# Kernel tuning notes

Hardware: AMD Instinct MI355X
Metric: run time of the kernel (lower is better)

## Reference

```python
import jax, jax.numpy as jnp
import numpy as np

K = 16          # neighbors used for attention (knn uses K+1 incl. self)
LRELU = 0.01    # torch LeakyReLU default negative_slope


def setup_inputs() -> dict:
    key = jax.random.key(0)
    ks = jax.random.split(key, 12)
    B, N = 4, 8192
    w = lambda k, shape: (jax.random.normal(k, shape, jnp.float32) * 0.05)
    inp = {
        "x": jax.random.normal(ks[0], (B, N, 3), jnp.float32),
        "global_feat": jax.random.normal(ks[1], (B, 1024), jnp.float32),  # unused by forward (matches source)
        # convs1 = MLP_CONV(3, [64,128]): Conv1d(3,64)+ReLU, Conv1d(64,128)
        "W1": w(ks[2], (64, 3)),    "b1": jnp.zeros((64,), jnp.float32),
        "W2": w(ks[3], (128, 64)),  "b2": jnp.zeros((128,), jnp.float32),
        # convs2: Conv2d(9,64,1x1)+LReLU, Conv2d(64,64,1x1)+LReLU, Conv2d(64,128,1x1)
        "Wc1": w(ks[4], (64, 9)),   "bc1": jnp.zeros((64,), jnp.float32),
        "Wc2": w(ks[5], (64, 64)),  "bc2": jnp.zeros((64,), jnp.float32),
        "Wc3": w(ks[6], (128, 64)), "bc3": jnp.zeros((128,), jnp.float32),
        # conv_query / conv_key: Conv2d(256,256,1x1)
        "Wq": w(ks[7], (256, 256)), "bq": jnp.zeros((256,), jnp.float32),
        "Wk": w(ks[8], (256, 256)), "bk": jnp.zeros((256,), jnp.float32),
    }
    return inp


def _lrelu(t):
    return jnp.where(t >= 0, t, LRELU * t)


def _forward(x, W1, b1, W2, b2, Wc1, bc1, Wc2, bc2, Wc3, bc3, Wq, bq, Wk, bk):
    # convs1: pointwise MLP on coords -> per-point features f [B,N,128]
    f = jax.nn.relu(jnp.einsum('bnc,oc->bno', x, W1) + b1)
    f = jnp.einsum('bnc,oc->bno', f, W2) + b2

    # knn_points(x, x, K=17): squared-distance matrix, nearest-first (self at slot 0)
    sq = jnp.sum(x * x, axis=-1)                              # [B,N]
    d2 = sq[:, :, None] + sq[:, None, :] - 2.0 * jnp.einsum('bnc,bmc->bnm', x, x)
    _, idx = jax.lax.top_k(-d2, K + 1)                        # [B,N,K+1]

    gather = jax.vmap(lambda a, i: a[i])                      # per-batch fancy gather
    knn_x = gather(x, idx)                                    # [B,N,K+1,3]
    knn_f = gather(f, idx)                                    # [B,N,K+1,128]

    rep = jnp.broadcast_to(x[:, :, None, :], knn_x.shape)     # repeat_x
    r = jnp.concatenate([rep, knn_x, rep - knn_x], axis=-1)   # [B,N,K+1,9]
    r = _lrelu(jnp.einsum('bnkc,oc->bnko', r, Wc1) + bc1)
    r = _lrelu(jnp.einsum('bnkc,oc->bnko', r, Wc2) + bc2)
    r = jnp.einsum('bnkc,oc->bnko', r, Wc3) + bc3             # [B,N,K+1,128]

    feat = jnp.concatenate([knn_f, r], axis=-1)               # [B,N,K+1,256]
    q = jnp.einsum('bnkc,oc->bnko', feat[:, :, :1, :], Wq) + bq   # [B,N,1,256]
    k = jnp.einsum('bnkc,oc->bnko', feat[:, :, 1:, :], Wk) + bk   # [B,N,K,256]
    w = jax.nn.softmax(jnp.sum(q * k, axis=-1), axis=-1)      # [B,N,K]
    new_x = jnp.sum(w[..., None] * knn_x[:, :, 1:, :], axis=2)    # [B,N,3]
    return new_x


def reference(x, global_feat, W1, b1, W2, b2, Wc1, bc1, Wc2, bc2, Wc3, bc3, Wq, bq, Wk, bk):
    del global_feat  # present in the torch signature but unused in forward
    return _forward(x, W1, b1, W2, b2, Wc1, bc1, Wc2, bc2, Wc3, bc3, Wq, bq, Wk, bk)
```

## Files before the change

kernel.cpp:

```cpp
#include <hip/hip_runtime.h>
#include <hip/hip_bf16.h>

#define NPTS 8192
#define NB   4

typedef unsigned short u16;
typedef unsigned int   u32;
typedef short bf16x8 __attribute__((ext_vector_type(8)));
typedef float f32x4  __attribute__((ext_vector_type(4)));

static __device__ __forceinline__ float bflo(u32 u){ return __uint_as_float(u << 16); }
static __device__ __forceinline__ float bfhi(u32 u){ return __uint_as_float(u & 0xffff0000u); }
static __device__ __forceinline__ u16 f2bf(float f){
  u32 x = __float_as_uint(f);
  return (u16)((x + 0x7fffu + ((x >> 16) & 1u)) >> 16);
}
static __device__ __forceinline__ float lrelu(float v){ return v >= 0.f ? v : 0.01f * v; }

__global__ __launch_bounds__(256) void k0_prep(const float* __restrict__ Wq, const float* __restrict__ bq,
                                               const float* __restrict__ Wk, const float* __restrict__ Wc3,
                                               const float* __restrict__ Wc2,
                                               u16* __restrict__ Mb, float* __restrict__ u,
                                               u16* __restrict__ Wc3T, u16* __restrict__ Wc2p){
  int oc = blockIdx.x, c = threadIdx.x;
  float acc = 0.f;
  for (int r = 0; r < 256; ++r) acc = fmaf(Wk[r*256 + oc], Wq[r*256 + c], acc);
  Mb[oc*256 + c] = f2bf(acc);
  __shared__ float red[256];
  red[c] = Wk[c*256 + oc] * bq[c];
  __syncthreads();
  for (int s = 128; s > 0; s >>= 1){ if (c < s) red[c] += red[c + s]; __syncthreads(); }
  if (c == 0) u[oc] = red[0];
  if (oc < 32){ int e = oc*256 + c; int h = e >> 7, o = e & 127; Wc3T[h*128 + o] = f2bf(Wc3[o*64 + h]); }
  if (oc >= 32 && oc < 48){ int e = (oc - 32)*256 + c; Wc2p[e] = f2bf(Wc2[e]); }
}

__global__ __launch_bounds__(128) void k1_feat(const float* __restrict__ x, const float* __restrict__ W1,
                                               const float* __restrict__ b1, const float* __restrict__ W2,
                                               const float* __restrict__ b2, u16* __restrict__ f){
  __shared__ float xs[16][4];
  __shared__ float hids[16][68];
  __shared__ float W2s[128][68];
  int b = blockIdx.y; int n0 = blockIdx.x * 16; int t = threadIdx.x;
  const float* xb = x + ((size_t)b*NPTS + n0)*3;
  if (t < 48){ int p = t/3, c = t - p*3; xs[p][c] = xb[p*3 + c]; }
  for (int e = t; e < 8192; e += 128) W2s[e >> 6][e & 63] = W2[e];
  __syncthreads();
  {
    int e = t;
    #pragma unroll
    for (int ii = 0; ii < 8; ++ii, e += 128){
      int p = e >> 6, h = e & 63;
      float v = b1[h];
      v = fmaf(W1[h*3+0], xs[p][0], v);
      v = fmaf(W1[h*3+1], xs[p][1], v);
      v = fmaf(W1[h*3+2], xs[p][2], v);
      hids[p][h] = v > 0.f ? v : 0.f;
    }
  }
  __syncthreads();
  int p = t >> 3, og = t & 7;
  float acc[16];
  #pragma unroll
  for (int i = 0; i < 16; ++i) acc[i] = b2[og + 8*i];
  #pragma unroll 4
  for (int c4 = 0; c4 < 16; ++c4){
    float4 hv = *(const float4*)&hids[p][c4*4];
    #pragma unroll
    for (int i = 0; i < 16; ++i){
      float4 wv = *(const float4*)&W2s[og + 8*i][c4*4];
      acc[i] = fmaf(wv.x, hv.x, acc[i]); acc[i] = fmaf(wv.y, hv.y, acc[i]);
      acc[i] = fmaf(wv.z, hv.z, acc[i]); acc[i] = fmaf(wv.w, hv.w, acc[i]);
    }
  }
  u16* fb = f + ((size_t)b*NPTS + n0)*128;
  #pragma unroll
  for (int i = 0; i < 16; ++i) fb[p*128 + og + 8*i] = f2bf(acc[i]);
}

#define K2_FLUSH8() do { \
    _Pragma("unroll") \
    for (int s = 0; s < 8; ++s){ \
      int2 pr = *(const int2*)(bufp + s*4096); \
      float d = (s < cnt) ? __int_as_float(pr.x) : __builtin_inff(); \
      int ii = pr.y; \
      bool pk = bd[16] > d; \
      _Pragma("unroll") \
      for (int k = 16; k >= 1; --k){ \
        bool pk1 = bd[k-1] > d; \
        float nd = pk1 ? bd[k-1] : d; \
        int   ni = pk1 ? bi[k-1] : ii; \
        if (pk){ bd[k] = nd; bi[k] = ni; } \
        pk = pk1; \
      } \
      if (pk){ bd[0] = d; bi[0] = ii; } \
    } \
    cnt = 0; } while (0)

__global__ __launch_bounds__(512) void k2_knn(const float* __restrict__ x, int* __restrict__ idxout){
#pragma clang fp contract(off)
  __shared__ __align__(16) char smem[52224];
  int t = threadIdx.x, lane = t & 63, w = t >> 6;
  int b = blockIdx.y;
  const float* xb = x + (size_t)b*NPTS*3;
  int q = blockIdx.x*64 + lane;
  float qx = xb[q*3+0], qy = xb[q*3+1], qz = xb[q*3+2];
  float qsq = (qx*qx + qy*qy) + qz*qz;
  float bd[17]; int bi[17];
  #pragma unroll
  for (int k = 0; k < 17; ++k){ bd[k] = __builtin_inff(); bi[k] = 0; }
  float4* tile = (float4*)smem;
  float*  tauv = (float*)(smem + 8192);
  char*   bufp = smem + 10240 + t*8;
  tauv[t] = __builtin_inff();
  __syncthreads();
  int cnt = 0;
  float gate = __builtin_inff();
  int c0 = w * 1024;
  for (int t0 = 0; t0 < 1024; t0 += 64){
    int m = c0 + t0 + lane;
    float cx = xb[m*3+0], cy = xb[m*3+1], cz = xb[m*3+2];
    float csq = (cx*cx + cy*cy) + cz*cz;
    tile[w*64 + lane] = make_float4(cx, cy, cz, csq);
    for (int j = 0; j < 64; ++j){
      float4 cd = tile[w*64 + j];
      float dt = (qx*cd.x + qy*cd.y) + qz*cd.z;
      float d2 = (qsq + cd.w) - 2.0f*dt;
      bool push = d2 < gate;
      if (__any(push)){
        if (push){
          *(int2*)(bufp + cnt*4096) = make_int2(__float_as_int(d2), c0 + t0 + j);
          ++cnt;
        }
        if (__any(cnt >= 8)){
          K2_FLUSH8();
          gate = fminf(gate, bd[16]);
        }
      }
    }
    tauv[t] = bd[16];
    float tm = fminf(tauv[lane], tauv[64 + lane]);
    tm = fminf(tm, fminf(tauv[128 + lane], tauv[192 + lane]));
    tm = fminf(tm, fminf(tauv[256 + lane], tauv[320 + lane]));
    tm = fminf(tm, fminf(tauv[384 + lane], tauv[448 + lane]));
    gate = fminf(tm, bd[16]);
  }
  K2_FLUSH8();
  __syncthreads();
  float* md   = (float*)smem;
  u16*   mi16 = (u16*)(smem + 34816);
  {
    int base = (w*64 + lane)*17;
    #pragma unroll
    for (int k = 0; k < 17; ++k){ md[base + k] = bd[k]; mi16[base + k] = (u16)bi[k]; }
  }
  __syncthreads();
  if (w == 0){
    int p0=0,p1=0,p2=0,p3=0,p4=0,p5=0,p6=0,p7=0;
    int* op = idxout + ((size_t)b*NPTS + q)*17;
    int base = lane*17;
    for (int k = 0; k < 17; ++k){
      float h0 = md[        base + p0];
      float h1 = md[1088  + base + p1];
      float h2 = md[2176  + base + p2];
      float h3 = md[3264  + base + p3];
      float h4 = md[4352  + base + p4];
      float h5 = md[5440  + base + p5];
      float h6 = md[6528  + base + p6];
      float h7 = md[7616  + base + p7];
      float best = h0; int ws = 0;
      if (h1 < best){ best = h1; ws = 1; }
      if (h2 < best){ best = h2; ws = 2; }
      if (h3 < best){ best = h3; ws = 3; }
      if (h4 < best){ best = h4; ws = 4; }
      if (h5 < best){ best = h5; ws = 5; }
      if (h6 < best){ best = h6; ws = 6; }
      if (h7 < best){ best = h7; ws = 7; }
      int pp = (ws==0)?p0:(ws==1)?p1:(ws==2)?p2:(ws==3)?p3:(ws==4)?p4:(ws==5)?p5:(ws==6)?p6:p7;
      op[k] = (int)mi16[ws*1088 + base + pp];
      p0 += (ws==0); p1 += (ws==1); p2 += (ws==2); p3 += (ws==3);
      p4 += (ws==4); p5 += (ws==5); p6 += (ws==6); p7 += (ws==7);
    }
  }
}

__global__ __launch_bounds__(256) void k3_qt(const float* __restrict__ x, const int* __restrict__ idx,
    const u16* __restrict__ f, const u16* __restrict__ Mb, const float* __restrict__ u,
    const u16* __restrict__ Wc3T,
    const float* __restrict__ Wc1, const float* __restrict__ bc1,
    const float* __restrict__ Wc2, const float* __restrict__ bc2,
    const float* __restrict__ bc3, float* __restrict__ qg){
  __shared__ __align__(16) char smem[73088];
  u16*   featb = (u16*)smem;
  float* qtBs  = (float*)(smem + 16896);
  float* h1s   = (float*)(smem + 16896);
  float* h2s   = (float*)(smem + 25600);
  float* Wc1s  = (float*)(smem + 34304);
  float* Wc2s  = (float*)(smem + 36608);
  u16*   W3sD  = (u16*)(smem + 36608);
  u16*   W3s   = (u16*)(smem + 54016);
  float* bcs   = (float*)(smem + 71424);
  float* xns   = (float*)(smem + 71936);
  float* xgs   = (float*)(smem + 72448);
  int*   idx0s = (int*)(smem + 72960);

  int b = blockIdx.y; int n0 = blockIdx.x * 32; int t = threadIdx.x;
  const int p3 = t >> 3, hg = t & 7;

  if (t < 32) idx0s[t] = idx[((size_t)b*NPTS + n0 + t)*17];
  {
    const float* xb = x + ((size_t)b*NPTS + n0)*3;
    if (t < 96){ int p = t/3, c = t - p*3; xns[p*4 + c] = xb[p*3 + c]; }
  }
  if (t < 128) bcs[t] = (t < 64) ? bc1[t] : bc2[t - 64];
  for (int e = t; e < 576; e += 256) Wc1s[e] = Wc1[e];
  for (int e = t; e < 4096; e += 256) Wc2s[(e >> 6)*68 + (e & 63)] = Wc2[e];
  __syncthreads();
  if (t < 96){ int p = t/3, c = t - p*3; xgs[p*4 + c] = x[((size_t)b*NPTS + idx0s[p])*3 + c]; }
  {
    int cg = t & 7;
    const uint4* fsrc = (const uint4*)(f + ((size_t)b*NPTS + idx0s[p3])*128) + cg*2;
    uint4 A = fsrc[0], B = fsrc[1];
    uint4* dst = (uint4*)&featb[p3*264 + cg*16];
    dst[0] = A; dst[1] = B;
  }
  __syncthreads();
  {
    float rv0 = xns[p3*4+0], rv1 = xns[p3*4+1], rv2 = xns[p3*4+2];
    float rv3 = xgs[p3*4+0], rv4 = xgs[p3*4+1], rv5 = xgs[p3*4+2];
    float rv6 = rv0 - rv3, rv7 = rv1 - rv4, rv8 = rv2 - rv5;
    #pragma unroll
    for (int i = 0; i < 8; ++i){
      int h = hg + 8*i;
      const float* wr = &Wc1s[h*9];
      float v = bcs[h];
      v = fmaf(wr[0], rv0, v); v = fmaf(wr[1], rv1, v); v = fmaf(wr[2], rv2, v);
      v = fmaf(wr[3], rv3, v); v = fmaf(wr[4], rv4, v); v = fmaf(wr[5], rv5, v);
      v = fmaf(wr[6], rv6, v); v = fmaf(wr[7], rv7, v); v = fmaf(wr[8], rv8, v);
      h1s[p3*68 + h] = lrelu(v);
    }
  }
  __syncthreads();
  {
    #pragma unroll
    for (int i = 0; i < 8; ++i){
      int h = hg + 8*i;
      float v = bcs[64 + h];
      const float* wr = &Wc2s[h*68];
      const float* ar = &h1s[p3*68];
      #pragma unroll
      for (int c4 = 0; c4 < 16; ++c4){
        float4 wv = *(const float4*)(wr + c4*4);
        float4 av = *(const float4*)(ar + c4*4);
        v = fmaf(wv.x, av.x, v); v = fmaf(wv.y, av.y, v);
        v = fmaf(wv.z, av.z, v); v = fmaf(wv.w, av.w, v);
      }
      h2s[p3*68 + h] = lrelu(v);
    }
  }
  __syncthreads();
  for (int e = t; e < 4096; e += 256) *(u32*)&W3s[(e >> 6)*136 + (e & 63)*2] = ((const u32*)Wc3T)[e];
  __syncthreads();
  {
    int og = hg;
    float4 a0 = *(const float4*)&bc3[og*16 + 0];
    float4 a1 = *(const float4*)&bc3[og*16 + 4];
    float4 a2 = *(const float4*)&bc3[og*16 + 8];
    float4 a3 = *(const float4*)&bc3[og*16 + 12];
    for (int h = 0; h < 64; ++h){
      float hv = h2s[p3*68 + h];
      const u32* wp = (const u32*)&W3s[h*136 + og*16];
      uint4 A = *(const uint4*)wp; uint4 B = *(const uint4*)(wp + 4);
      a0.x = fmaf(bflo(A.x), hv, a0.x); a0.y = fmaf(bfhi(A.x), hv, a0.y);
      a0.z = fmaf(bflo(A.y), hv, a0.z); a0.w = fmaf(bfhi(A.y), hv, a0.w);
      a1.x = fmaf(bflo(A.z), hv, a1.x); a1.y = fmaf(bfhi(A.z), hv, a1.y);
      a1.z = fmaf(bflo(A.w), hv, a1.z); a1.w = fmaf(bfhi(A.w), hv, a1.w);
      a2.x = fmaf(bflo(B.x), hv, a2.x); a2.y = fmaf(bfhi(B.x), hv, a2.y);
      a2.z = fmaf(bflo(B.y), hv, a2.z); a2.w = fmaf(bfhi(B.y), hv, a2.w);
      a3.x = fmaf(bflo(B.z), hv, a3.x); a3.y = fmaf(bfhi(B.z), hv, a3.y);
      a3.z = fmaf(bflo(B.w), hv, a3.z); a3.w = fmaf(bfhi(B.w), hv, a3.w);
    }
    u16* dst = &featb[p3*264 + 128 + og*16];
    u32 pw[8];
    pw[0] = (u32)f2bf(a0.x) | ((u32)f2bf(a0.y) << 16);
    pw[1] = (u32)f2bf(a0.z) | ((u32)f2bf(a0.w) << 16);
    pw[2] = (u32)f2bf(a1.x) | ((u32)f2bf(a1.y) << 16);
    pw[3] = (u32)f2bf(a1.z) | ((u32)f2bf(a1.w) << 16);
    pw[4] = (u32)f2bf(a2.x) | ((u32)f2bf(a2.y) << 16);
    pw[5] = (u32)f2bf(a2.z) | ((u32)f2bf(a2.w) << 16);
    pw[6] = (u32)f2bf(a3.x) | ((u32)f2bf(a3.y) << 16);
    pw[7] = (u32)f2bf(a3.z) | ((u32)f2bf(a3.w) << 16);
    ((uint4*)dst)[0] = make_uint4(pw[0], pw[1], pw[2], pw[3]);
    ((uint4*)dst)[1] = make_uint4(pw[4], pw[5], pw[6], pw[7]);
  }
  __syncthreads();
  {
    int lane = t & 63, wv = t >> 6;
    int l15 = lane & 15, kq = lane >> 4;
    f32x4 acc[2][4];
    #pragma unroll
    for (int rt = 0; rt < 2; ++rt)
      #pragma unroll
      for (int ct = 0; ct < 4; ++ct)
        acc[rt][ct] = (f32x4){0.f, 0.f, 0.f, 0.f};
    #pragma unroll
    for (int ks = 0; ks < 8; ++ks){
      bf16x8 a0 = *(const bf16x8*)&featb[l15*264 + ks*32 + kq*8];
      bf16x8 a1 = *(const bf16x8*)&featb[(16 + l15)*264 + ks*32 + kq*8];
      #pragma unroll
      for (int ct = 0; ct < 4; ++ct){
        int oc = wv*64 + ct*16 + l15;
        bf16x8 bb = *(const bf16x8*)(Mb + oc*256 + ks*32 + kq*8);
        acc[0][ct] = __builtin_amdgcn_mfma_f32_16x16x32_bf16(a0, bb, acc[0][ct], 0, 0, 0);
        acc[1][ct] = __builtin_amdgcn_mfma_f32_16x16x32_bf16(a1, bb, acc[1][ct], 0, 0, 0);
      }
    }
    if (wv < 2){
      float* qgb = qg + ((size_t)b*NPTS + n0)*192;
      #pragma unroll
      for (int ct = 0; ct < 4; ++ct){
        int oc = wv*64 + ct*16 + l15;
        float uv = u[oc];
        #pragma unroll
        for (int rt = 0; rt < 2; ++rt){
          #pragma unroll
          for (int j = 0; j < 4; ++j){
            int p = rt*16 + kq*4 + j;
            qgb[(size_t)p*192 + oc] = acc[rt][ct][j] + uv;
          }
        }
      }
    } else {
      #pragma unroll
      for (int ct = 0; ct < 4; ++ct){
        int oc = (wv - 2)*64 + ct*16 + l15;
        float uv = u[128 + oc];
        #pragma unroll
        for (int rt = 0; rt < 2; ++rt){
          #pragma unroll
          for (int j = 0; j < 4; ++j){
            int p = rt*16 + kq*4 + j;
            qtBs[p*132 + oc] = acc[rt][ct][j] + uv;
          }
        }
      }
    }
  }
  __syncthreads();
  for (int e = t; e < 4096; e += 256) *(u32*)&W3sD[(e >> 6)*136 + (e & 63)*2] = ((const u32*)Wc3T)[e];
  __syncthreads();
  {
    float gacc[8];
    #pragma unroll
    for (int i = 0; i < 8; ++i) gacc[i] = 0.f;
    for (int o8 = 0; o8 < 16; ++o8){
      const float* qr = &qtBs[p3*132 + o8*8];
      float4 qa = *(const float4*)qr; float4 qb4 = *(const float4*)(qr + 4);
      #pragma unroll
      for (int i = 0; i < 8; ++i){
        int h = hg + 8*i;
        const uint4 WU = *(const uint4*)&W3sD[h*136 + o8*8];
        float acc = gacc[i];
        acc = fmaf(bflo(WU.x), qa.x, acc); acc = fmaf(bfhi(WU.x), qa.y, acc);
        acc = fmaf(bflo(WU.y), qa.z, acc); acc = fmaf(bfhi(WU.y), qa.w, acc);
        acc = fmaf(bflo(WU.z), qb4.x, acc); acc = fmaf(bfhi(WU.z), qb4.y, acc);
        acc = fmaf(bflo(WU.w), qb4.z, acc); acc = fmaf(bfhi(WU.w), qb4.w, acc);
        gacc[i] = acc;
      }
    }
    float* qgb = qg + ((size_t)b*NPTS + n0)*192;
    #pragma unroll
    for (int i = 0; i < 8; ++i) qgb[p3*192 + 128 + hg + 8*i] = gacc[i];
  }
}

__global__ __launch_bounds__(256) void k4_attn(const float* __restrict__ x, const int* __restrict__ idx,
    const u16* __restrict__ f, const float* __restrict__ qg,
    const float* __restrict__ Wc1, const float* __restrict__ bc1,
    const float* __restrict__ bc2, const u16* __restrict__ Wc2p,
    float* __restrict__ out){
  __shared__ int   idxs[16][17];
  __shared__ float xns[16][4];
  __shared__ float qgs[16][196];
  __shared__ float Wc1s[576];
  __shared__ float bcs[128];
  __shared__ float xjs[256][4];
  __shared__ float flog[256];
  __shared__ u16   h1t[256][76];
  int b = blockIdx.y; int n0 = blockIdx.x * 16; int t = threadIdx.x;
  for (int e = t; e < 272; e += 256){ int p = e/17, k = e - p*17; idxs[p][k] = idx[((size_t)b*NPTS + n0 + p)*17 + k]; }
  if (t < 48){ int p = t/3, c = t - p*3; xns[p][c] = x[((size_t)b*NPTS + n0 + p)*3 + c]; }
  if (t < 128) bcs[t] = (t < 64) ? bc1[t] : bc2[t - 64];
  for (int e = t; e < 576; e += 256) Wc1s[e] = Wc1[e];
  {
    const float* src = qg + ((size_t)b*NPTS + n0)*192;
    for (int e = t; e < 3072; e += 256){ int p = e/192, c = e - p*192; qgs[p][c] = src[e]; }
  }
  __syncthreads();
  {
    int p = t >> 4, j = t & 15;
    int nidx = idxs[p][j + 1];
    const float* xr = x + ((size_t)b*NPTS + nidx)*3;
    float cx = xr[0], cy = xr[1], cz = xr[2];
    *(float4*)&xjs[t][0] = make_float4(cx, cy, cz, 0.f);
    float rx = xns[p][0], ry = xns[p][1], rz = xns[p][2];
    float dx = rx - cx, dy = ry - cy, dz = rz - cz;
    float logit = 0.f;
    {
      const u32* fr = (const u32*)(f + ((size_t)b*NPTS + nidx)*128);
      #pragma unroll
      for (int c8 = 0; c8 < 16; ++c8){
        uint4 FU = *(const uint4*)(fr + c8*4);
        const float* qr = &qgs[p][c8*8];
        float4 qa = *(const float4*)qr; float4 qb4 = *(const float4*)(qr + 4);
        logit = fmaf(bflo(FU.x), qa.x, logit); logit = fmaf(bfhi(FU.x), qa.y, logit);
        logit = fmaf(bflo(FU.y), qa.z, logit); logit = fmaf(bfhi(FU.y), qa.w, logit);
        logit = fmaf(bflo(FU.z), qb4.x, logit); logit = fmaf(bfhi(FU.z), qb4.y, logit);
        logit = fmaf(bflo(FU.w), qb4.z, logit); logit = fmaf(bfhi(FU.w), qb4.w, logit);
      }
    }
    flog[t] = logit;
    float h1r[64];
    #pragma unroll
    for (int h = 0; h < 64; ++h){
      const float* wr = &Wc1s[h*9];
      float v = bcs[h];
      v = fmaf(wr[0], rx, v); v = fmaf(wr[1], ry, v); v = fmaf(wr[2], rz, v);
      v = fmaf(wr[3], cx, v); v = fmaf(wr[4], cy, v); v = fmaf(wr[5], cz, v);
      v = fmaf(wr[6], dx, v); v = fmaf(wr[7], dy, v); v = fmaf(wr[8], dz, v);
      h1r[h] = lrelu(v);
    }
    u16* hrow = &h1t[t][0];
    #pragma unroll
    for (int c8 = 0; c8 < 8; ++c8){
      u32 w0 = (u32)f2bf(h1r[c8*8+0]) | ((u32)f2bf(h1r[c8*8+1]) << 16);
      u32 w1 = (u32)f2bf(h1r[c8*8+2]) | ((u32)f2bf(h1r[c8*8+3]) << 16);
      u32 w2 = (u32)f2bf(h1r[c8*8+4]) | ((u32)f2bf(h1r[c8*8+5]) << 16);
      u32 w3 = (u32)f2bf(h1r[c8*8+6]) | ((u32)f2bf(h1r[c8*8+7]) << 16);
      *(uint4*)&hrow[c8*8] = make_uint4(w0, w1, w2, w3);
    }
  }
  __syncthreads();
  {
    int lane = t & 63, wv = t >> 6;
    int l15 = lane & 15, kq = lane >> 4;
    f32x4 acc[4][4];
    #pragma unroll
    for (int rt = 0; rt < 4; ++rt)
      #pragma unroll
      for (int ct = 0; ct < 4; ++ct)
        acc[rt][ct] = (f32x4){0.f, 0.f, 0.f, 0.f};
    #pragma unroll
    for (int ks = 0; ks < 2; ++ks){
      bf16x8 av[4];
      #pragma unroll
      for (int rt = 0; rt < 4; ++rt)
        av[rt] = *(const bf16x8*)&h1t[wv*64 + rt*16 + l15][ks*32 + kq*8];
      #pragma unroll
      for (int ct = 0; ct < 4; ++ct){
        bf16x8 bv = *(const bf16x8*)(Wc2p + (ct*16 + l15)*64 + ks*32 + kq*8);
        #pragma unroll
        for (int rt = 0; rt < 4; ++rt)
          acc[rt][ct] = __builtin_amdgcn_mfma_f32_16x16x32_bf16(av[rt], bv, acc[rt][ct], 0, 0, 0);
      }
    }
    float lg[4][4];
    #pragma unroll
    for (int rt = 0; rt < 4; ++rt)
      #pragma unroll
      for (int reg = 0; reg < 4; ++reg) lg[rt][reg] = 0.f;
    #pragma unroll
    for (int ct = 0; ct < 4; ++ct){
      int col = ct*16 + l15;
      float b2v = bcs[64 + col];
      #pragma unroll
      for (int rt = 0; rt < 4; ++rt){
        float gv = qgs[wv*4 + rt][128 + col];
        #pragma unroll
        for (int reg = 0; reg < 4; ++reg){
          float h2 = lrelu(acc[rt][ct][reg] + b2v);
          lg[rt][reg] = fmaf(gv, h2, lg[rt][reg]);
        }
      }
    }
    #pragma unroll
    for (int s = 1; s < 16; s <<= 1){
      #pragma unroll
      for (int rt = 0; rt < 4; ++rt)
        #pragma unroll
        for (int reg = 0; reg < 4; ++reg)
          lg[rt][reg] += __shfl_xor(lg[rt][reg], s, 64);
    }
    #pragma unroll
    for (int rt = 0; rt < 4; ++rt){
      float4 fl = *(const float4*)&flog[(wv*4 + rt)*16 + kq*4];
      float l0 = lg[rt][0] + fl.x, l1 = lg[rt][1] + fl.y;
      float l2 = lg[rt][2] + fl.z, l3 = lg[rt][3] + fl.w;
      float mx = fmaxf(fmaxf(l0, l1), fmaxf(l2, l3));
      mx = fmaxf(mx, __shfl_xor(mx, 16, 64));
      mx = fmaxf(mx, __shfl_xor(mx, 32, 64));
      float e0 = expf(l0 - mx), e1 = expf(l1 - mx), e2 = expf(l2 - mx), e3 = expf(l3 - mx);
      float sm = (e0 + e1) + (e2 + e3);
      sm += __shfl_xor(sm, 16, 64);
      sm += __shfl_xor(sm, 32, 64);
      int rbase = (wv*4 + rt)*16 + kq*4;
      float4 x0 = *(const float4*)&xjs[rbase + 0][0];
      float4 x1 = *(const float4*)&xjs[rbase + 1][0];
      float4 x2 = *(const float4*)&xjs[rbase + 2][0];
      float4 x3 = *(const float4*)&xjs[rbase + 3][0];
      float ox = e0*x0.x + e1*x1.x + e2*x2.x + e3*x3.x;
      float oy = e0*x0.y + e1*x1.y + e2*x2.y + e3*x3.y;
      float oz = e0*x0.z + e1*x1.z + e2*x2.z + e3*x3.z;
      ox += __shfl_xor(ox, 16, 64); ox += __shfl_xor(ox, 32, 64);
      oy += __shfl_xor(oy, 16, 64); oy += __shfl_xor(oy, 32, 64);
      oz += __shfl_xor(oz, 16, 64); oz += __shfl_xor(oz, 32, 64);
      if (kq == 0 && l15 == rt){
        float inv = 1.f / sm;
        float* op = out + ((size_t)b*NPTS + n0 + wv*4 + rt)*3;
        op[0] = ox * inv; op[1] = oy * inv; op[2] = oz * inv;
      }
    }
  }
}

extern "C" void kernel_launch(void* const* d_in, const int* in_sizes, int n_in,
                              void* d_out, int out_size, void* d_ws, size_t ws_size,
                              hipStream_t stream){
  (void)in_sizes; (void)n_in; (void)out_size; (void)ws_size;
  const float* x   = (const float*)d_in[0];
  const float* W1  = (const float*)d_in[2];
  const float* b1  = (const float*)d_in[3];
  const float* W2  = (const float*)d_in[4];
  const float* b2  = (const float*)d_in[5];
  const float* Wc1 = (const float*)d_in[6];
  const float* bc1 = (const float*)d_in[7];
  const float* Wc2 = (const float*)d_in[8];
  const float* bc2 = (const float*)d_in[9];
  const float* Wc3 = (const float*)d_in[10];
  const float* bc3 = (const float*)d_in[11];
  const float* Wq  = (const float*)d_in[12];
  const float* bq  = (const float*)d_in[13];
  const float* Wk  = (const float*)d_in[14];
  float* out = (float*)d_out;

  char* ws = (char*)d_ws;
  u16*   Mb   = (u16*)(ws + 0);
  float* u    = (float*)(ws + 131072);
  u16*   Wc3T = (u16*)(ws + 132096);
  u16*   Wc2p = (u16*)(ws + 153600);
  u16*   fbuf = (u16*)(ws + (1u << 20));
  int*   idxb = (int*)(ws + (16u << 20));
  float* qgb  = (float*)(ws + (32u << 20));

  k0_prep<<<dim3(256), dim3(256), 0, stream>>>(Wq, bq, Wk, Wc3, Wc2, Mb, u, Wc3T, Wc2p);
  k1_feat<<<dim3(512, NB), dim3(128), 0, stream>>>(x, W1, b1, W2, b2, fbuf);
  k2_knn<<<dim3(128, NB), dim3(512), 0, stream>>>(x, idxb);
  k3_qt<<<dim3(256, NB), dim3(256), 0, stream>>>(x, idxb, fbuf, Mb, u, Wc3T, Wc1, bc1, Wc2, bc2, bc3, qgb);
  k4_attn<<<dim3(512, NB), dim3(256), 0, stream>>>(x, idxb, fbuf, qgb, Wc1, bc1, bc2, Wc2p, out);
}
```

Measured before the change: 444.1 us.

## Sort points by x-coordinate and prune KNN candidate tiles by x-distance bound

```diff
diff --git a/kernel.cpp b/kernel.cpp
--- a/kernel.cpp
+++ b/kernel.cpp
@@ -6,6 +6,7 @@
 
 typedef unsigned short u16;
 typedef unsigned int   u32;
+typedef unsigned long long u64;
 typedef short bf16x8 __attribute__((ext_vector_type(8)));
 typedef float f32x4  __attribute__((ext_vector_type(4)));
 
@@ -76,6 +77,45 @@
   u16* fb = f + ((size_t)b*NPTS + n0)*128;
   #pragma unroll
   for (int i = 0; i < 16; ++i) fb[p*128 + og + 8*i] = f2bf(acc[i]);
+}
+
+__global__ __launch_bounds__(1024) void k2s_sort(const float* __restrict__ x,
+                                                 float4* __restrict__ xs4,
+                                                 u32* __restrict__ perm){
+#pragma clang fp contract(off)
+  __shared__ u64 a[8192];
+  int b = blockIdx.x, t = threadIdx.x;
+  const float* xb = x + (size_t)b*NPTS*3;
+  for (int i = t; i < 8192; i += 1024){
+    u32 kb = __float_as_uint(xb[i*3]);
+    kb = (kb & 0x80000000u) ? ~kb : (kb | 0x80000000u);
+    a[i] = ((u64)kb << 32) | (u32)i;
+  }
+  __syncthreads();
+  for (int k = 2; k <= 8192; k <<= 1){
+    for (int j = k >> 1; j > 0; j >>= 1){
+      #pragma clang loop unroll_count(1)
+      for (int i = t; i < 8192; i += 1024){
+        int ixj = i ^ j;
+        if (ixj > i){
+          u64 ai = a[i], aj = a[ixj];
+          bool up = ((i & k) == 0);
+          bool sw = up ? (ai > aj) : (ai < aj);
+          if (sw){ a[i] = aj; a[ixj] = ai; }
+        }
+      }
+      __syncthreads();
+    }
+  }
+  float4* xs4b = xs4 + (size_t)b*NPTS;
+  u32* permb = perm + (size_t)b*NPTS;
+  for (int i = t; i < 8192; i += 1024){
+    u32 orig = (u32)(a[i] & 0xFFFFFFFFu);
+    float cx = xb[orig*3+0], cy = xb[orig*3+1], cz = xb[orig*3+2];
+    float csq = (cx*cx + cy*cy) + cz*cz;
+    xs4b[i] = make_float4(cx, cy, cz, csq);
+    permb[i] = orig;
+  }
 }
 
 #define K2_FLUSH8() do { \
@@ -97,15 +137,25 @@
     } \
     cnt = 0; } while (0)
 
-__global__ __launch_bounds__(512) void k2_knn(const float* __restrict__ x, int* __restrict__ idxout){
+#define K2_GATE() do { \
+    tauv[t] = bd[16]; \
+    float tm = fminf(tauv[lane], tauv[64 + lane]); \
+    tm = fminf(tm, fminf(tauv[128 + lane], tauv[192 + lane])); \
+    tm = fminf(tm, fminf(tauv[256 + lane], tauv[320 + lane])); \
+    tm = fminf(tm, fminf(tauv[384 + lane], tauv[448 + lane])); \
+    gate = fminf(tm, bd[16]); } while (0)
+
+__global__ __launch_bounds__(512) void k2_knn(const float4* __restrict__ xs4,
+                                              const u32* __restrict__ perm,
+                                              int* __restrict__ idxout){
 #pragma clang fp contract(off)
   __shared__ __align__(16) char smem[52224];
   int t = threadIdx.x, lane = t & 63, w = t >> 6;
   int b = blockIdx.y;
-  const float* xb = x + (size_t)b*NPTS*3;
-  int q = blockIdx.x*64 + lane;
-  float qx = xb[q*3+0], qy = xb[q*3+1], qz = xb[q*3+2];
-  float qsq = (qx*qx + qy*qy) + qz*qz;
+  const float4* xsb = xs4 + (size_t)b*NPTS;
+  int Q0 = blockIdx.x*64;
+  float4 qv = xsb[Q0 + lane];
+  float qx = qv.x, qy = qv.y, qz = qv.z, qsq = qv.w;
   float bd[17]; int bi[17];
   #pragma unroll
   for (int k = 0; k < 17; ++k){ bd[k] = __builtin_inff(); bi[k] = 0; }
@@ -116,12 +166,18 @@
   __syncthreads();
   int cnt = 0;
   float gate = __builtin_inff();
-  int c0 = w * 1024;
-  for (int t0 = 0; t0 < 1024; t0 += 64){
-    int m = c0 + t0 + lane;
-    float cx = xb[m*3+0], cy = xb[m*3+1], cz = xb[m*3+2];
-    float csq = (cx*cx + cy*cy) + cz*cz;
-    tile[w*64 + lane] = make_float4(cx, cy, cz, csq);
+  int T, Tstep;
+  if (w < 4){ T = blockIdx.x + w;           Tstep = 4; }
+  else      { T = blockIdx.x - 1 - (w - 4); Tstep = -4; }
+  for (; (unsigned)T < 128u; T += Tstep){
+    float4 cq = xsb[T*64 + lane];
+    tile[w*64 + lane] = cq;
+    float edge = __shfl(cq.x, (Tstep > 0) ? 0 : 63, 64);
+    float dxe = edge - qx;
+    bool prune = (Tstep > 0) ? (dxe > 0.f && dxe*dxe >= gate)
+                             : (dxe < 0.f && dxe*dxe >= gate);
+    if (__all(prune)) break;
+    int cb = T*64;
     for (int j = 0; j < 64; ++j){
       float4 cd = tile[w*64 + j];
       float dt = (qx*cd.x + qy*cd.y) + qz*cd.z;
@@ -129,21 +185,16 @@
       bool push = d2 < gate;
       if (__any(push)){
         if (push){
-          *(int2*)(bufp + cnt*4096) = make_int2(__float_as_int(d2), c0 + t0 + j);
+          *(int2*)(bufp + cnt*4096) = make_int2(__float_as_int(d2), cb + j);
           ++cnt;
         }
         if (__any(cnt >= 8)){
           K2_FLUSH8();
-          gate = fminf(gate, bd[16]);
+          K2_GATE();
         }
       }
     }
-    tauv[t] = bd[16];
-    float tm = fminf(tauv[lane], tauv[64 + lane]);
-    tm = fminf(tm, fminf(tauv[128 + lane], tauv[192 + lane]));
-    tm = fminf(tm, fminf(tauv[256 + lane], tauv[320 + lane]));
-    tm = fminf(tm, fminf(tauv[384 + lane], tauv[448 + lane]));
-    gate = fminf(tm, bd[16]);
+    K2_GATE();
   }
   K2_FLUSH8();
   __syncthreads();
@@ -156,8 +207,9 @@
   }
   __syncthreads();
   if (w == 0){
+    const u32* permb = perm + (size_t)b*NPTS;
     int p0=0,p1=0,p2=0,p3=0,p4=0,p5=0,p6=0,p7=0;
-    int* op = idxout + ((size_t)b*NPTS + q)*17;
+    int* op = idxout + ((size_t)b*NPTS + permb[Q0 + lane])*17;
     int base = lane*17;
     for (int k = 0; k < 17; ++k){
       float h0 = md[        base + p0];
@@ -177,7 +229,7 @@
       if (h6 < best){ best = h6; ws = 6; }
       if (h7 < best){ best = h7; ws = 7; }
       int pp = (ws==0)?p0:(ws==1)?p1:(ws==2)?p2:(ws==3)?p3:(ws==4)?p4:(ws==5)?p5:(ws==6)?p6:p7;
-      op[k] = (int)mi16[ws*1088 + base + pp];
+      op[k] = (int)permb[(u32)mi16[ws*1088 + base + pp]];
       p0 += (ws==0); p1 += (ws==1); p2 += (ws==2); p3 += (ws==3);
       p4 += (ws==4); p5 += (ws==5); p6 += (ws==6); p7 += (ws==7);
     }
@@ -550,11 +602,14 @@
   u16*   Wc2p = (u16*)(ws + 153600);
   u16*   fbuf = (u16*)(ws + (1u << 20));
   int*   idxb = (int*)(ws + (16u << 20));
+  float4* xs4 = (float4*)(ws + (20u << 20));
+  u32*   perm = (u32*)(ws + (24u << 20));
   float* qgb  = (float*)(ws + (32u << 20));
 
   k0_prep<<<dim3(256), dim3(256), 0, stream>>>(Wq, bq, Wk, Wc3, Wc2, Mb, u, Wc3T, Wc2p);
+  k2s_sort<<<dim3(NB), dim3(1024), 0, stream>>>(x, xs4, perm);
   k1_feat<<<dim3(512, NB), dim3(128), 0, stream>>>(x, W1, b1, W2, b2, fbuf);
-  k2_knn<<<dim3(128, NB), dim3(512), 0, stream>>>(x, idxb);
+  k2_knn<<<dim3(128, NB), dim3(512), 0, stream>>>(xs4, perm, idxb);
   k3_qt<<<dim3(256, NB), dim3(256), 0, stream>>>(x, idxb, fbuf, Mb, u, Wc3T, Wc1, bc1, Wc2, bc2, bc3, qgb);
   k4_attn<<<dim3(512, NB), dim3(256), 0, stream>>>(x, idxb, fbuf, qgb, Wc1, bc1, bc2, Wc2p, out);
 }
```

New measurement: 569.4 us. +28.2%, slower.
